# Kernel optimization log

Hardware: AMD Instinct MI355X
Metric: run time of the kernel (lower is better)

The kernel has to match this reference:

```python
import jax, jax.numpy as jnp
import numpy as np

B, S, H, I, E, K = 2, 512, 768, 3072, 8, 1
LB_COEF = 0.01


def _xavier(key, shape, fan_in, fan_out):
    limit = np.sqrt(6.0 / (fan_in + fan_out)).astype(np.float32)
    return jax.random.uniform(key, shape, jnp.float32, -limit, limit)


def setup_inputs() -> dict:
    key = jax.random.key(0)
    k0, k1, k2, k3 = jax.random.split(key, 4)
    return {
        "hidden_states": jax.random.normal(k0, (B, S, H), jnp.float32),
        "gate_w": _xavier(k1, (E, H), H, E),          # nn.Linear(H, E).weight
        "gate_b": jnp.zeros((E,), jnp.float32),
        "w1": _xavier(k2, (E, I, H), H, I),           # per-expert Linear(H, I).weight
        "b1": jnp.zeros((E, I), jnp.float32),
        "w2": _xavier(k3, (E, H, I), I, H),           # per-expert Linear(I, H).weight
        "b2": jnp.zeros((E, H), jnp.float32),
    }


def reference(hidden_states, gate_w, gate_b, w1, b1, w2, b2):
    b, s, h = hidden_states.shape
    x = hidden_states.reshape(-1, h)                      # [T, H]
    gate_logits = x @ gate_w.T + gate_b                   # [T, E]
    top_vals, top_idx = jax.lax.top_k(gate_logits, K)     # [T, K]
    # softmax over the (single) selected logit in fp32 -> all ones, kept for fidelity
    gate_weights = jax.nn.softmax(top_vals.astype(jnp.float32), axis=-1)  # [T, K]

    # load balancing loss (torch.var is unbiased, ddof=1)
    gate_mean = gate_logits.mean(axis=0)                  # [E]
    gate_var = gate_logits.var(axis=0, ddof=1)            # [E]
    lb_loss = LB_COEF * (gate_var / (gate_mean ** 2 + 1e-8)).mean()

    # dense per-expert FFN (exact math; combine picks the routed expert)
    hmid = jnp.einsum('th,eih->tei', x, w1) + b1          # [T, E, I]
    hmid = jax.nn.gelu(hmid, approximate=False)           # torch nn.GELU (erf)
    y = jnp.einsum('tei,ehi->teh', hmid, w2) + b2         # [T, E, H]

    sel = top_idx[:, 0]                                   # [T]
    y_sel = jnp.take_along_axis(y, sel[:, None, None], axis=1)[:, 0]  # [T, H]
    out = y_sel * gate_weights[:, 0:1]                    # weight == 1.0 for k=1
    return out.reshape(b, s, h), lb_loss
```

## Files before the change

kernel.cpp:

```cpp
#include <hip/hip_runtime.h>
#include <hip/hip_bf16.h>
#include <math.h>

#define Hdim 768
#define Idim 3072
#define Tn   1024
#define En   8
#define CAP  256
#define LD2  136

using v4f     = __attribute__((ext_vector_type(4))) float;
using short8  = __attribute__((ext_vector_type(8))) short;
using short4v = __attribute__((ext_vector_type(4))) short;

__device__ inline unsigned short f2bf(float f) {
    unsigned u = __float_as_uint(f);
    u += 0x7fffu + ((u >> 16) & 1u);
    return (unsigned short)(u >> 16);
}
__device__ inline short4v pack4(float4 v) {
    return short4v{ (short)f2bf(v.x), (short)f2bf(v.y), (short)f2bf(v.z), (short)f2bf(v.w) };
}
__device__ __forceinline__ void gl2lds16(const unsigned short* g, unsigned short* l) {
    __builtin_amdgcn_global_load_lds(
        (const __attribute__((address_space(1))) void*)g,
        (__attribute__((address_space(3))) void*)l, 16, 0, 0);
}

__global__ __launch_bounds__(256) void gate_kernel(
    const float* __restrict__ x, const float* __restrict__ gw, const float* __restrict__ gb,
    float* __restrict__ psum, float* __restrict__ psumsq,
    int* __restrict__ sel, int* __restrict__ gcur)
{
    __shared__ float gws[8 * 772];
    __shared__ float lg[8][8];
    int tid = threadIdx.x;
    long t0 = (long)blockIdx.x * 8;
    if (blockIdx.x == 0 && tid < En) gcur[tid] = 0;
    for (int i = tid; i < 8 * 768; i += 256) gws[(i / 768) * 772 + (i % 768)] = gw[i];
    __syncthreads();

    int tok = tid >> 5, e = (tid >> 2) & 7, qr = tid & 3;
    const float4* xp = (const float4*)(x + (t0 + tok) * Hdim) + qr * 48;
    const float4* gp = (const float4*)(gws + e * 772) + qr * 48;
    float a0 = 0.f, a1 = 0.f;
#pragma unroll 8
    for (int i = 0; i < 48; i += 2) {
        float4 xa = xp[i], ga = gp[i], xc = xp[i + 1], gc = gp[i + 1];
        a0 += xa.x * ga.x + xa.y * ga.y + xa.z * ga.z + xa.w * ga.w;
        a1 += xc.x * gc.x + xc.y * gc.y + xc.z * gc.z + xc.w * gc.w;
    }
    float acc = a0 + a1;
    acc += __shfl_xor(acc, 1);
    acc += __shfl_xor(acc, 2);
    if (qr == 0) lg[tok][e] = acc + gb[e];
    __syncthreads();

    if (tid < 8) {
        float best = lg[tid][0]; int bi = 0;
        for (int j = 1; j < 8; j++) { float v = lg[tid][j]; if (v > best) { best = v; bi = j; } }
        sel[t0 + tid] = bi;
    } else if (tid < 16) {
        int e2 = tid - 8;
        float s = 0.f, ss = 0.f;
        for (int t2 = 0; t2 < 8; t2++) { float v = lg[t2][e2]; s += v; ss += v * v; }
        psum[blockIdx.x * 8 + e2]   = s;
        psumsq[blockIdx.x * 8 + e2] = ss;
    }
}

__global__ __launch_bounds__(256) void gather_kernel(
    const float* __restrict__ x, const int* __restrict__ sel,
    const float* __restrict__ psum, const float* __restrict__ psumsq,
    int* __restrict__ gcur, int* __restrict__ perm,
    unsigned short* __restrict__ xb, float* __restrict__ out_lb)
{
    int tid = threadIdx.x;
    if (blockIdx.x == 0 && tid < 64) {
        int e = tid & 7, c0 = (tid >> 3) * 16;
        float s = 0.f, ss = 0.f;
        for (int b = c0; b < c0 + 16; b++) { s += psum[b * 8 + e]; ss += psumsq[b * 8 + e]; }
        s  += __shfl_xor(s, 8);  s  += __shfl_xor(s, 16);  s  += __shfl_xor(s, 32);
        ss += __shfl_xor(ss, 8); ss += __shfl_xor(ss, 16); ss += __shfl_xor(ss, 32);
        if (tid < 8) {
            float mean = s * (1.0f / 1024.0f);
            float var  = (ss - s * mean) * (1.0f / 1023.0f);
            float r = var / (mean * mean + 1e-8f);
            r += __shfl_xor(r, 1); r += __shfl_xor(r, 2); r += __shfl_xor(r, 4);
            if (tid == 0) out_lb[0] = 0.01f * r * 0.125f;
        }
    }
    int t = blockIdx.x * 4 + (tid >> 6);
    int lane = tid & 63;
    int e = sel[t];
    int pos = 0;
    if (lane == 0) pos = atomicAdd(&gcur[e], 1);
    pos = __shfl(pos, 0);
    if (pos < CAP) {
        int slot = (e << 8) + pos;
        if (lane == 0) perm[slot] = t;
        const float4* src = (const float4*)(x + (long)t * Hdim);
        unsigned short* dst = xb + (long)slot * Hdim;
#pragma unroll
        for (int i = 0; i < 3; i++) {
            int c = lane + 64 * i;
            *(short4v*)(dst + c * 4) = pack4(src[c]);
        }
    }
}

__global__ __launch_bounds__(256) void gemm1_kernel(
    const unsigned short* __restrict__ xb, const float* __restrict__ w1, const float* __restrict__ b1,
    const int* __restrict__ count, unsigned short* __restrict__ hmid)
{
    int e = blockIdx.z;
    int nloc = count[e]; if (nloc > CAP) nloc = CAP;
    int m0 = blockIdx.y << 6;
    if (m0 >= nloc) return;
    int n0 = blockIdx.x << 5;
    int off = e << 8;

    __shared__ __align__(16) unsigned short As[64 * 128];
    __shared__ __align__(16) unsigned short Bs[32 * LD2];

    int tid = threadIdx.x;
    int lane = tid & 63, wave = tid >> 6;
    int quad = lane >> 4, l16 = lane & 15;
    int wm = wave << 4;

    const unsigned short* aG[4];
    unsigned short* aL[4];
#pragma unroll
    for (int i = 0; i < 4; i++) {
        int p = (wave * 4 + i) * 64 + lane;
        int row = p >> 4;
        int kc = (p & 15) ^ (row & 15);
        int m = m0 + row; int mm = m < nloc ? m : nloc - 1;
        aG[i] = xb + (long)(off + mm) * Hdim + kc * 8;
        aL[i] = (unsigned short*)As + p * 8;
    }
    int kq5 = tid & 31, rb8 = tid >> 5;
    const float* bp[4];
#pragma unroll
    for (int s = 0; s < 4; s++)
        bp[s] = w1 + ((long)e * Idim + n0 + rb8 + 8 * s) * Hdim + kq5 * 4;

    v4f acc[2];
    acc[0] = (v4f){0.f, 0.f, 0.f, 0.f};
    acc[1] = (v4f){0.f, 0.f, 0.f, 0.f};

    float4 nb[4];
#pragma unroll
    for (int s = 0; s < 4; s++) nb[s] = *(const float4*)bp[s];

    for (int kb = 0; kb < Hdim; kb += 128) {
        __syncthreads();
#pragma unroll
        for (int i = 0; i < 4; i++) gl2lds16(aG[i] + kb, aL[i]);
#pragma unroll
        for (int s = 0; s < 4; s++)
            *(short4v*)(Bs + (rb8 + 8 * s) * LD2 + kq5 * 4) = pack4(nb[s]);
        __syncthreads();
        if (kb + 128 < Hdim) {
#pragma unroll
            for (int s = 0; s < 4; s++) nb[s] = *(const float4*)(bp[s] + kb + 128);
        }
#pragma unroll
        for (int s = 0; s < 4; s++) {
            int r = wm + l16;
            short8 af = *(const short8*)(As + r * 128 + (((s * 4 + quad) ^ (r & 15)) * 8));
            short8 bf2[2];
#pragma unroll
            for (int j = 0; j < 2; j++)
                bf2[j] = *(const short8*)(Bs + (j * 16 + l16) * LD2 + s * 32 + quad * 8);
#pragma unroll
            for (int j = 0; j < 2; j++)
                acc[j] = __builtin_amdgcn_mfma_f32_16x16x32_bf16(af, bf2[j], acc[j], 0, 0, 0);
        }
    }

    int mr = wm + quad * 4;
#pragma unroll
    for (int r = 0; r < 4; r++) {
        int m = m0 + mr + r;
        if (m >= nloc) continue;
        long slot = off + m;
#pragma unroll
        for (int j = 0; j < 2; j++) {
            int n = n0 + j * 16 + l16;
            float v = acc[j][r] + b1[e * Idim + n];
            float g = 0.5f * v * (1.0f + erff(v * 0.70710678118654752f));
            hmid[slot * Idim + n] = f2bf(g);
        }
    }
}

__global__ __launch_bounds__(256) void gemm2_kernel(
    const unsigned short* __restrict__ hmid, const float* __restrict__ w2,
    const int* __restrict__ count, const int* __restrict__ perm,
    float* __restrict__ parts)
{
    int e = blockIdx.z;
    int nloc = count[e]; if (nloc > CAP) nloc = CAP;
    int m0 = blockIdx.y << 6;
    if (m0 >= nloc) return;
    int bx = blockIdx.x;
    int n0 = (bx % 24) << 5;
    int kc4 = bx / 24;
    long kbase = (long)kc4 * 768;
    int off = e << 8;

    __shared__ __align__(16) unsigned short As[64 * 128];
    __shared__ __align__(16) unsigned short Bs[32 * LD2];

    int tid = threadIdx.x;
    int lane = tid & 63, wave = tid >> 6;
    int quad = lane >> 4, l16 = lane & 15;
    int wm = wave << 4;

    const unsigned short* aG[4];
    unsigned short* aL[4];
#pragma unroll
    for (int i = 0; i < 4; i++) {
        int p = (wave * 4 + i) * 64 + lane;
        int row = p >> 4;
        int kc = (p & 15) ^ (row & 15);
        int m = m0 + row; int mm = m < nloc ? m : nloc - 1;
        aG[i] = hmid + (long)(off + mm) * Idim + kbase + kc * 8;
        aL[i] = (unsigned short*)As + p * 8;
    }
    int kq5 = tid & 31, rb8 = tid >> 5;
    const float* bp[4];
#pragma unroll
    for (int s = 0; s < 4; s++)
        bp[s] = w2 + ((long)e * Hdim + n0 + rb8 + 8 * s) * Idim + kbase + kq5 * 4;

    v4f acc[2];
    acc[0] = (v4f){0.f, 0.f, 0.f, 0.f};
    acc[1] = (v4f){0.f, 0.f, 0.f, 0.f};

    float4 nb[4];
#pragma unroll
    for (int s = 0; s < 4; s++) nb[s] = *(const float4*)bp[s];

    for (int kb = 0; kb < 768; kb += 128) {
        __syncthreads();
#pragma unroll
        for (int i = 0; i < 4; i++) gl2lds16(aG[i] + kb, aL[i]);
#pragma unroll
        for (int s = 0; s < 4; s++)
            *(short4v*)(Bs + (rb8 + 8 * s) * LD2 + kq5 * 4) = pack4(nb[s]);
        __syncthreads();
        if (kb + 128 < 768) {
#pragma unroll
            for (int s = 0; s < 4; s++) nb[s] = *(const float4*)(bp[s] + kb + 128);
        }
#pragma unroll
        for (int s = 0; s < 4; s++) {
            int r = wm + l16;
            short8 af = *(const short8*)(As + r * 128 + (((s * 4 + quad) ^ (r & 15)) * 8));
            short8 bf2[2];
#pragma unroll
            for (int j = 0; j < 2; j++)
                bf2[j] = *(const short8*)(Bs + (j * 16 + l16) * LD2 + s * 32 + quad * 8);
#pragma unroll
            for (int j = 0; j < 2; j++)
                acc[j] = __builtin_amdgcn_mfma_f32_16x16x32_bf16(af, bf2[j], acc[j], 0, 0, 0);
        }
    }

    float* pout = parts + (long)kc4 * Tn * Hdim;
    int mr = wm + quad * 4;
#pragma unroll
    for (int r = 0; r < 4; r++) {
        int m = m0 + mr + r;
        if (m >= nloc) continue;
        int t = perm[off + m];
#pragma unroll
        for (int j = 0; j < 2; j++) {
            int n = n0 + j * 16 + l16;
            pout[(long)t * Hdim + n] = acc[j][r];
        }
    }
}

__global__ __launch_bounds__(256) void reduce_kernel(
    const float* __restrict__ parts, const float* __restrict__ b2,
    const int* __restrict__ sel, float* __restrict__ out)
{
    int idx = blockIdx.x * 256 + threadIdx.x;
    int t = idx / 192, n4 = idx - t * 192;
    int e = sel[t];
    const float4* p = (const float4*)parts;
    float4 a = p[idx];
    float4 b = p[idx + 196608];
    float4 c = p[idx + 2 * 196608];
    float4 d = p[idx + 3 * 196608];
    float4 bias = ((const float4*)(b2 + (long)e * Hdim))[n4];
    float4 r;
    r.x = a.x + b.x + c.x + d.x + bias.x;
    r.y = a.y + b.y + c.y + d.y + bias.y;
    r.z = a.z + b.z + c.z + d.z + bias.z;
    r.w = a.w + b.w + c.w + d.w + bias.w;
    ((float4*)out)[idx] = r;
}

extern "C" void kernel_launch(void* const* d_in, const int* in_sizes, int n_in,
                              void* d_out, int out_size, void* d_ws, size_t ws_size,
                              hipStream_t stream)
{
    const float* x  = (const float*)d_in[0];
    const float* gw = (const float*)d_in[1];
    const float* gb = (const float*)d_in[2];
    const float* w1 = (const float*)d_in[3];
    const float* b1 = (const float*)d_in[4];
    const float* w2 = (const float*)d_in[5];
    const float* b2 = (const float*)d_in[6];
    float* out = (float*)d_out;

    int*   gcur   = (int*)d_ws;
    int*   sel    = (int*)((char*)d_ws + 128);
    float* psum   = (float*)((char*)d_ws + 4352);
    float* psumsq = (float*)((char*)d_ws + 8448);
    int*   perm   = (int*)((char*)d_ws + 12544);
    unsigned short* xb   = (unsigned short*)((char*)d_ws + 32768);
    unsigned short* hmid = (unsigned short*)((char*)d_ws + (1u << 22));
    float* parts = (float*)((char*)d_ws + (1u << 25));

    gate_kernel  <<<128, 256, 0, stream>>>(x, gw, gb, psum, psumsq, sel, gcur);
    gather_kernel<<<256, 256, 0, stream>>>(x, sel, psum, psumsq, gcur, perm, xb,
                                           out + (long)Tn * Hdim);
    gemm1_kernel <<<dim3(96, 4, 8), 256, 0, stream>>>(xb, w1, b1, gcur, hmid);
    gemm2_kernel <<<dim3(96, 4, 8), 256, 0, stream>>>(hmid, w2, gcur, perm, parts);
    reduce_kernel<<<768, 256, 0, stream>>>(parts, b2, sel, out);
}
```

Before: 236.5 us.

## Load A fragments directly to registers and double-buffer B tiles in both GEMMs

Both expert GEMM kernels stop staging the activation tile through LDS with global_load_lds. Each wave now loads its A fragments straight from global memory into registers, and the converted weight tile goes into a two-stage LDS ping-pong buffer with a two-deep register prefetch. Each k-step now needs one barrier instead of two, and s_setprio is raised around the MFMA section, all meant to overlap weight loads with compute. In exchange register pressure rises, and A rows are no longer shared through LDS, so reads depend on cache locality.

New measurement: 248.3 us. +5.0%, slower.

```diff
diff --git a/kernel.cpp b/kernel.cpp
--- a/kernel.cpp
+++ b/kernel.cpp
@@ -20,11 +20,6 @@
 }
 __device__ inline short4v pack4(float4 v) {
     return short4v{ (short)f2bf(v.x), (short)f2bf(v.y), (short)f2bf(v.z), (short)f2bf(v.w) };
-}
-__device__ __forceinline__ void gl2lds16(const unsigned short* g, unsigned short* l) {
-    __builtin_amdgcn_global_load_lds(
-        (const __attribute__((address_space(1))) void*)g,
-        (__attribute__((address_space(3))) void*)l, 16, 0, 0);
 }
 
 __global__ __launch_bounds__(256) void gate_kernel(
@@ -120,62 +115,70 @@
     int n0 = blockIdx.x << 5;
     int off = e << 8;
 
-    __shared__ __align__(16) unsigned short As[64 * 128];
-    __shared__ __align__(16) unsigned short Bs[32 * LD2];
+    __shared__ __align__(16) unsigned short Bs[2][32 * LD2];
 
     int tid = threadIdx.x;
     int lane = tid & 63, wave = tid >> 6;
     int quad = lane >> 4, l16 = lane & 15;
     int wm = wave << 4;
 
-    const unsigned short* aG[4];
-    unsigned short* aL[4];
-#pragma unroll
-    for (int i = 0; i < 4; i++) {
-        int p = (wave * 4 + i) * 64 + lane;
-        int row = p >> 4;
-        int kc = (p & 15) ^ (row & 15);
-        int m = m0 + row; int mm = m < nloc ? m : nloc - 1;
-        aG[i] = xb + (long)(off + mm) * Hdim + kc * 8;
-        aL[i] = (unsigned short*)As + p * 8;
-    }
+    int arow = m0 + wm + l16; if (arow >= nloc) arow = nloc - 1;
+    const unsigned short* ap = xb + (long)(off + arow) * Hdim + quad * 8;
+
     int kq5 = tid & 31, rb8 = tid >> 5;
     const float* bp[4];
 #pragma unroll
     for (int s = 0; s < 4; s++)
         bp[s] = w1 + ((long)e * Idim + n0 + rb8 + 8 * s) * Hdim + kq5 * 4;
+    unsigned short* bw = &Bs[0][0] + rb8 * LD2 + kq5 * 4;
+    const unsigned short* brd0 = &Bs[0][0] + l16 * LD2 + quad * 8;
 
     v4f acc[2];
     acc[0] = (v4f){0.f, 0.f, 0.f, 0.f};
     acc[1] = (v4f){0.f, 0.f, 0.f, 0.f};
 
-    float4 nb[4];
-#pragma unroll
-    for (int s = 0; s < 4; s++) nb[s] = *(const float4*)bp[s];
-
-    for (int kb = 0; kb < Hdim; kb += 128) {
-        __syncthreads();
-#pragma unroll
-        for (int i = 0; i < 4; i++) gl2lds16(aG[i] + kb, aL[i]);
-#pragma unroll
-        for (int s = 0; s < 4; s++)
-            *(short4v*)(Bs + (rb8 + 8 * s) * LD2 + kq5 * 4) = pack4(nb[s]);
-        __syncthreads();
-        if (kb + 128 < Hdim) {
-#pragma unroll
-            for (int s = 0; s < 4; s++) nb[s] = *(const float4*)(bp[s] + kb + 128);
-        }
+    short8 aF[2][4];
+    float4 nbv[2][4];
+#pragma unroll
+    for (int s = 0; s < 4; s++) nbv[0][s] = *(const float4*)(bp[s]);
+#pragma unroll
+    for (int s = 0; s < 4; s++) aF[0][s] = *(const short8*)(ap + s * 32);
+#pragma unroll
+    for (int s = 0; s < 4; s++) nbv[1][s] = *(const float4*)(bp[s] + 128);
+#pragma unroll
+    for (int s = 0; s < 4; s++) aF[1][s] = *(const short8*)(ap + 128 + s * 32);
+#pragma unroll
+    for (int s = 0; s < 4; s++) *(short4v*)(bw + s * 8 * LD2) = pack4(nbv[0][s]);
+    asm volatile("s_waitcnt lgkmcnt(0)" ::: "memory");
+    __builtin_amdgcn_s_barrier();
+    __builtin_amdgcn_sched_barrier(0);
+
+#pragma unroll
+    for (int t = 0; t < 6; t++) {
+        const int par = t & 1, nxt = par ^ 1;
+        const unsigned short* brd = brd0 + par * 32 * LD2;
+        __builtin_amdgcn_s_setprio(1);
 #pragma unroll
         for (int s = 0; s < 4; s++) {
-            int r = wm + l16;
-            short8 af = *(const short8*)(As + r * 128 + (((s * 4 + quad) ^ (r & 15)) * 8));
-            short8 bf2[2];
-#pragma unroll
-            for (int j = 0; j < 2; j++)
-                bf2[j] = *(const short8*)(Bs + (j * 16 + l16) * LD2 + s * 32 + quad * 8);
-#pragma unroll
-            for (int j = 0; j < 2; j++)
-                acc[j] = __builtin_amdgcn_mfma_f32_16x16x32_bf16(af, bf2[j], acc[j], 0, 0, 0);
+            short8 bfa = *(const short8*)(brd + s * 32);
+            short8 bfb = *(const short8*)(brd + 16 * LD2 + s * 32);
+            acc[0] = __builtin_amdgcn_mfma_f32_16x16x32_bf16(aF[par][s], bfa, acc[0], 0, 0, 0);
+            acc[1] = __builtin_amdgcn_mfma_f32_16x16x32_bf16(aF[par][s], bfb, acc[1], 0, 0, 0);
+        }
+        __builtin_amdgcn_s_setprio(0);
+        if (t + 2 < 6) {
+#pragma unroll
+            for (int s = 0; s < 4; s++) nbv[par][s] = *(const float4*)(bp[s] + (t + 2) * 128);
+#pragma unroll
+            for (int s = 0; s < 4; s++) aF[par][s] = *(const short8*)(ap + (t + 2) * 128 + s * 32);
+        }
+        if (t + 1 < 6) {
+            unsigned short* bwn = bw + nxt * 32 * LD2;
+#pragma unroll
+            for (int s = 0; s < 4; s++) *(short4v*)(bwn + s * 8 * LD2) = pack4(nbv[nxt][s]);
+            asm volatile("s_waitcnt lgkmcnt(0)" ::: "memory");
+            __builtin_amdgcn_s_barrier();
+            __builtin_amdgcn_sched_barrier(0);
         }
     }
 
@@ -210,62 +213,70 @@
     long kbase = (long)kc4 * 768;
     int off = e << 8;
 
-    __shared__ __align__(16) unsigned short As[64 * 128];
-    __shared__ __align__(16) unsigned short Bs[32 * LD2];
+    __shared__ __align__(16) unsigned short Bs[2][32 * LD2];
 
     int tid = threadIdx.x;
     int lane = tid & 63, wave = tid >> 6;
     int quad = lane >> 4, l16 = lane & 15;
     int wm = wave << 4;
 
-    const unsigned short* aG[4];
-    unsigned short* aL[4];
-#pragma unroll
-    for (int i = 0; i < 4; i++) {
-        int p = (wave * 4 + i) * 64 + lane;
-        int row = p >> 4;
-        int kc = (p & 15) ^ (row & 15);
-        int m = m0 + row; int mm = m < nloc ? m : nloc - 1;
-        aG[i] = hmid + (long)(off + mm) * Idim + kbase + kc * 8;
-        aL[i] = (unsigned short*)As + p * 8;
-    }
+    int arow = m0 + wm + l16; if (arow >= nloc) arow = nloc - 1;
+    const unsigned short* ap = hmid + (long)(off + arow) * Idim + kbase + quad * 8;
+
     int kq5 = tid & 31, rb8 = tid >> 5;
     const float* bp[4];
 #pragma unroll
     for (int s = 0; s < 4; s++)
         bp[s] = w2 + ((long)e * Hdim + n0 + rb8 + 8 * s) * Idim + kbase + kq5 * 4;
+    unsigned short* bw = &Bs[0][0] + rb8 * LD2 + kq5 * 4;
+    const unsigned short* brd0 = &Bs[0][0] + l16 * LD2 + quad * 8;
 
     v4f acc[2];
     acc[0] = (v4f){0.f, 0.f, 0.f, 0.f};
     acc[1] = (v4f){0.f, 0.f, 0.f, 0.f};
 
-    float4 nb[4];
-#pragma unroll
-    for (int s = 0; s < 4; s++) nb[s] = *(const float4*)bp[s];
-
-    for (int kb = 0; kb < 768; kb += 128) {
-        __syncthreads();
-#pragma unroll
-        for (int i = 0; i < 4; i++) gl2lds16(aG[i] + kb, aL[i]);
-#pragma unroll
-        for (int s = 0; s < 4; s++)
-            *(short4v*)(Bs + (rb8 + 8 * s) * LD2 + kq5 * 4) = pack4(nb[s]);
-        __syncthreads();
-        if (kb + 128 < 768) {
-#pragma unroll
-            for (int s = 0; s < 4; s++) nb[s] = *(const float4*)(bp[s] + kb + 128);
-        }
+    short8 aF[2][4];
+    float4 nbv[2][4];
+#pragma unroll
+    for (int s = 0; s < 4; s++) nbv[0][s] = *(const float4*)(bp[s]);
+#pragma unroll
+    for (int s = 0; s < 4; s++) aF[0][s] = *(const short8*)(ap + s * 32);
+#pragma unroll
+    for (int s = 0; s < 4; s++) nbv[1][s] = *(const float4*)(bp[s] + 128);
+#pragma unroll
+    for (int s = 0; s < 4; s++) aF[1][s] = *(const short8*)(ap + 128 + s * 32);
+#pragma unroll
+    for (int s = 0; s < 4; s++) *(short4v*)(bw + s * 8 * LD2) = pack4(nbv[0][s]);
+    asm volatile("s_waitcnt lgkmcnt(0)" ::: "memory");
+    __builtin_amdgcn_s_barrier();
+    __builtin_amdgcn_sched_barrier(0);
+
+#pragma unroll
+    for (int t = 0; t < 6; t++) {
+        const int par = t & 1, nxt = par ^ 1;
+        const unsigned short* brd = brd0 + par * 32 * LD2;
+        __builtin_amdgcn_s_setprio(1);
 #pragma unroll
         for (int s = 0; s < 4; s++) {
-            int r = wm + l16;
-            short8 af = *(const short8*)(As + r * 128 + (((s * 4 + quad) ^ (r & 15)) * 8));
-            short8 bf2[2];
-#pragma unroll
-            for (int j = 0; j < 2; j++)
-                bf2[j] = *(const short8*)(Bs + (j * 16 + l16) * LD2 + s * 32 + quad * 8);
-#pragma unroll
-            for (int j = 0; j < 2; j++)
-                acc[j] = __builtin_amdgcn_mfma_f32_16x16x32_bf16(af, bf2[j], acc[j], 0, 0, 0);
+            short8 bfa = *(const short8*)(brd + s * 32);
+            short8 bfb = *(const short8*)(brd + 16 * LD2 + s * 32);
+            acc[0] = __builtin_amdgcn_mfma_f32_16x16x32_bf16(aF[par][s], bfa, acc[0], 0, 0, 0);
+            acc[1] = __builtin_amdgcn_mfma_f32_16x16x32_bf16(aF[par][s], bfb, acc[1], 0, 0, 0);
+        }
+        __builtin_amdgcn_s_setprio(0);
+        if (t + 2 < 6) {
+#pragma unroll
+            for (int s = 0; s < 4; s++) nbv[par][s] = *(const float4*)(bp[s] + (t + 2) * 128);
+#pragma unroll
+            for (int s = 0; s < 4; s++) aF[par][s] = *(const short8*)(ap + (t + 2) * 128 + s * 32);
+        }
+        if (t + 1 < 6) {
+            unsigned short* bwn = bw + nxt * 32 * LD2;
+#pragma unroll
+            for (int s = 0; s < 4; s++) *(short4v*)(bwn + s * 8 * LD2) = pack4(nbv[nxt][s]);
+            asm volatile("s_waitcnt lgkmcnt(0)" ::: "memory");
+            __builtin_amdgcn_s_barrier();
+            __builtin_amdgcn_sched_barrier(0);
         }
     }
 
```
